# Kernel tuning notes

Measured on AMD Instinct MI355X. Metric: run time of the kernel, lower is better.

The kernel has to match this reference:

```python
import jax, jax.numpy as jnp
import numpy as np

B, L, D, H, U = 1024, 256, 256, 512, 512


def setup_inputs() -> dict:
    key = jax.random.key(0)
    ks = jax.random.split(key, 5)
    scale_f = 1.0
    return {
        "features": jax.random.normal(ks[0], (B, L, D), dtype=jnp.float32),
        "hidden": jax.random.normal(ks[1], (B, H), dtype=jnp.float32),
        "W1": jax.random.normal(ks[2], (D, U), dtype=jnp.float32) / np.sqrt(D),
        "b1": jnp.zeros((U,), dtype=jnp.float32),
        "W2": jax.random.normal(ks[3], (H, U), dtype=jnp.float32) / np.sqrt(H),
        "b2": jnp.zeros((U,), dtype=jnp.float32),
        "Wv": jax.random.normal(ks[4], (U, 1), dtype=jnp.float32) / np.sqrt(U),
        "bv": jnp.zeros((1,), dtype=jnp.float32),
    }


def reference(features, hidden, W1, b1, W2, b2, Wv, bv):
    # features: [B, L, D], hidden: [B, H]
    proj_f = jnp.einsum("bld,du->blu", features, W1) + b1      # [B, L, U]
    proj_h = (hidden @ W2 + b2)[:, None, :]                      # [B, 1, U]
    score = jnp.tanh(proj_f + proj_h)                            # [B, L, U]
    logits = jnp.einsum("blu,uo->blo", score, Wv) + bv           # [B, L, 1]
    attention_weights = jax.nn.softmax(logits, axis=1)           # [B, L, 1]
    context_vector = jnp.sum(attention_weights * features, axis=1)  # [B, D]
    return (context_vector, attention_weights)
```

## Files before the change

### kernel.cpp

```cpp
#include <hip/hip_runtime.h>
#include <hip/hip_bf16.h>

#define B_ 1024
#define L_ 256
#define D_ 256
#define H_ 512
#define U_ 512
#define M_ (B_ * L_)

#define BM 128
#define BN 128
#define BK 64

typedef float f32x4 __attribute__((ext_vector_type(4)));
typedef short bf16x8 __attribute__((ext_vector_type(8)));

__device__ __forceinline__ short f2bf(float f) {
  unsigned u = __float_as_uint(f);
  u += 0x7fffu + ((u >> 16) & 1u);
  return (short)(u >> 16);
}

__device__ __forceinline__ void load16_g2l(const void* g, void* l) {
  __builtin_amdgcn_global_load_lds(
      (const __attribute__((address_space(1))) unsigned int*)g,
      (__attribute__((address_space(3))) unsigned int*)l, 16, 0, 0);
}

__device__ __forceinline__ float fast_tanh(float x) {
  float e = __expf(2.0f * x);
  return 1.0f - 2.0f * __builtin_amdgcn_rcpf(e + 1.0f);
}

__global__ void k_w1t(const float* __restrict__ W1, short* __restrict__ W1T) {
  int idx = blockIdx.x * 256 + threadIdx.x;
  int u = idx >> 8;
  int d = idx & 255;
  W1T[idx] = f2bf(W1[(size_t)d * U_ + u]);
}

__global__ void k_projh(const float* __restrict__ hidden, const float* __restrict__ W2,
                        const float* __restrict__ b1, const float* __restrict__ b2,
                        float* __restrict__ ph) {
  int u = blockIdx.x * 256 + threadIdx.x;
  int b0 = blockIdx.y * 8;
  float acc[8] = {0.f, 0.f, 0.f, 0.f, 0.f, 0.f, 0.f, 0.f};
  for (int h = 0; h < H_; ++h) {
    float w = W2[(size_t)h * U_ + u];
#pragma unroll
    for (int i = 0; i < 8; ++i) acc[i] = fmaf(hidden[(size_t)(b0 + i) * H_ + h], w, acc[i]);
  }
  float bias = b1[u] + b2[u];
#pragma unroll
  for (int i = 0; i < 8; ++i) ph[(size_t)(b0 + i) * U_ + u] = acc[i] + bias;
}

__global__ __launch_bounds__(256, 3) void k_gemm(
    const float* __restrict__ F,
    const short* __restrict__ W1T,
    const float* __restrict__ ph,
    const float* __restrict__ Wv,
    float* __restrict__ logits) {
  __shared__ __align__(16) short As[BM * BK];
  __shared__ __align__(16) short Bs[2][BN * BK];

  const int tid = threadIdx.x;
  const int lane = tid & 63;
  const int hi = lane >> 4;
  const int wid = tid >> 6;
  const int wr = wid >> 1, wc = wid & 1;
  const int tile = ((blockIdx.x & 7) << 10) | (blockIdx.x >> 3);
  const int ntile = tile & 3;
  const int mtile = tile >> 2;
  const int m0 = mtile * BM;
  const int n0 = ntile * BN;
  const int b = m0 >> 8;

  const bf16x8* As8 = (const bf16x8*)As;

  const float* agp[4];
  int aslot[4];
  const short* bgp[4];
#pragma unroll
  for (int i = 0; i < 4; ++i) {
    int s = i * 256 + tid;
    int arow = s >> 3;
    int akq = (s & 7) ^ (arow & 7);
    agp[i] = F + (size_t)(m0 + arow) * D_ + akq * 8;
    aslot[i] = s;
    bgp[i] = W1T + (size_t)(n0 + arow) * D_ + akq * 8;
  }

  f32x4 acc[4][4];
  const f32x4 fz = {0.f, 0.f, 0.f, 0.f};
#pragma unroll
  for (int mi = 0; mi < 4; ++mi)
#pragma unroll
    for (int ni = 0; ni < 4; ++ni) acc[mi][ni] = fz;

  f32x4 ar[4][2];
#pragma unroll
  for (int i = 0; i < 4; ++i) {
    ar[i][0] = *(const f32x4*)(agp[i]);
    ar[i][1] = *(const f32x4*)(agp[i] + 4);
    agp[i] += BK;
  }
#pragma unroll
  for (int i = 0; i < 4; ++i) {
    load16_g2l(bgp[i], &Bs[0][(size_t)(i * 256 + tid) * 8]);
    bgp[i] += BK;
  }

  for (int kt = 0; kt < 4; ++kt) {
    const bf16x8* BsC = (const bf16x8*)Bs[kt & 1];
    __syncthreads();
#pragma unroll
    for (int i = 0; i < 4; ++i) {
      bf16x8 w;
#pragma unroll
      for (int j = 0; j < 4; ++j) { w[j] = f2bf(ar[i][0][j]); w[4 + j] = f2bf(ar[i][1][j]); }
      ((bf16x8*)As)[aslot[i]] = w;
    }
    __syncthreads();
    if (kt < 3) {
#pragma unroll
      for (int i = 0; i < 4; ++i) {
        ar[i][0] = *(const f32x4*)(agp[i]);
        ar[i][1] = *(const f32x4*)(agp[i] + 4);
        agp[i] += BK;
      }
#pragma unroll
      for (int i = 0; i < 4; ++i) {
        load16_g2l(bgp[i], &Bs[(kt + 1) & 1][(size_t)(i * 256 + tid) * 8]);
        bgp[i] += BK;
      }
    }

#pragma unroll
    for (int kk = 0; kk < 2; ++kk) {
      bf16x8 af[4], bfr[4];
#pragma unroll
      for (int mi = 0; mi < 4; ++mi) {
        int rA = wr * 64 + mi * 16 + (lane & 15);
        af[mi] = As8[rA * 8 + ((kk * 4 + hi) ^ (rA & 7))];
      }
#pragma unroll
      for (int ni = 0; ni < 4; ++ni) {
        int nB = wc * 64 + ni * 16 + (lane & 15);
        bfr[ni] = BsC[nB * 8 + ((kk * 4 + hi) ^ (nB & 7))];
      }
#pragma unroll
      for (int mi = 0; mi < 4; ++mi)
#pragma unroll
        for (int ni = 0; ni < 4; ++ni)
          acc[mi][ni] = __builtin_amdgcn_mfma_f32_16x16x32_bf16(af[mi], bfr[ni], acc[mi][ni], 0, 0, 0);
    }
  }

  const float* phr = ph + (size_t)b * U_;
  float phv[4], wvv[4];
#pragma unroll
  for (int ni = 0; ni < 4; ++ni) {
    int u = n0 + wc * 64 + ni * 16 + (lane & 15);
    phv[ni] = phr[u];
    wvv[ni] = Wv[u];
  }
#pragma unroll
  for (int mi = 0; mi < 4; ++mi) {
    float cs[4] = {0.f, 0.f, 0.f, 0.f};
#pragma unroll
    for (int ni = 0; ni < 4; ++ni) {
#pragma unroll
      for (int r = 0; r < 4; ++r) {
        float x = acc[mi][ni][r] + phv[ni];
        cs[r] += fast_tanh(x) * wvv[ni];
      }
    }
#pragma unroll
    for (int off = 1; off < 16; off <<= 1) {
#pragma unroll
      for (int r = 0; r < 4; ++r) cs[r] += __shfl_xor(cs[r], off);
    }
    if ((lane & 15) == 0) {
      int g = m0 + wr * 64 + mi * 16 + ((lane >> 4) << 2);
#pragma unroll
      for (int r = 0; r < 4; ++r) atomicAdd(&logits[g + r], cs[r]);
    }
  }
}

__global__ void k_smctx(const float* __restrict__ logits, const float* __restrict__ F,
                        float* __restrict__ outw, float* __restrict__ ctx) {
  __shared__ float wl[L_];
  __shared__ f32x4 part[256];
  __shared__ float red[8];
  int b = blockIdx.x, t = threadIdx.x;
  float x = logits[(size_t)b * L_ + t];
  float m = x;
#pragma unroll
  for (int off = 32; off >= 1; off >>= 1) m = fmaxf(m, __shfl_xor(m, off));
  if ((t & 63) == 0) red[t >> 6] = m;
  __syncthreads();
  m = fmaxf(fmaxf(red[0], red[1]), fmaxf(red[2], red[3]));
  float e = __expf(x - m);
  float s = e;
#pragma unroll
  for (int off = 32; off >= 1; off >>= 1) s += __shfl_xor(s, off);
  if ((t & 63) == 0) red[4 + (t >> 6)] = s;
  __syncthreads();
  s = (red[4] + red[5]) + (red[6] + red[7]);
  float w = e / s;
  outw[(size_t)b * L_ + t] = w;
  wl[t] = w;
  __syncthreads();

  int lq = t >> 6, dq = t & 63;
  const f32x4* F4 = (const f32x4*)(F + (size_t)b * L_ * D_);
  f32x4 acc = {0.f, 0.f, 0.f, 0.f};
  for (int l = lq; l < L_; l += 4) acc += wl[l] * F4[l * 64 + dq];
  part[t] = acc;
  __syncthreads();
  if (lq == 0) {
    f32x4 r = (part[t] + part[t + 64]) + (part[t + 128] + part[t + 192]);
    ((f32x4*)ctx)[(size_t)b * 64 + dq] = r;
  }
}

extern "C" void kernel_launch(void* const* d_in, const int* in_sizes, int n_in,
                              void* d_out, int out_size, void* d_ws, size_t ws_size,
                              hipStream_t stream) {
  const float* F      = (const float*)d_in[0];
  const float* hidden = (const float*)d_in[1];
  const float* W1     = (const float*)d_in[2];
  const float* b1     = (const float*)d_in[3];
  const float* W2     = (const float*)d_in[4];
  const float* b2     = (const float*)d_in[5];
  const float* Wv     = (const float*)d_in[6];

  float* out_ctx = (float*)d_out;
  float* out_w   = out_ctx + (size_t)B_ * D_;

  char* ws = (char*)d_ws;
  short* W1T   = (short*)ws;
  float* ph    = (float*)(ws + 262144);
  float* logits = (float*)(ws + 262144 + 2097152);

  hipMemsetAsync(logits, 0, (size_t)M_ * sizeof(float), stream);
  k_w1t<<<512, 256, 0, stream>>>(W1, W1T);
  k_projh<<<dim3(2, 128), 256, 0, stream>>>(hidden, W2, b1, b2, ph);
  k_gemm<<<8192, 256, 0, stream>>>(F, W1T, ph, Wv, logits);
  k_smctx<<<1024, 256, 0, stream>>>(logits, F, out_w, out_ctx);
}
```

Measured before the change: 236.5 us.

## Pre-cast features to bf16 in a separate pass and load GEMM A tiles via direct-to-LDS

Adds a kernel that converts the full fp32 feature tensor to bf16 in workspace. The GEMM then loads both A and B tiles with global_load_lds, drops register staging and the in-kernel conversion, and single-buffers B so it can run at higher occupancy (launch bounds 4). In exchange it adds an extra full read of F plus a bf16 write and re-read (about 128 MB and 64 MB of traffic), and the K loop no longer prefetches the next tile. The old kernel is kept as a fallback when the workspace is too small for the bf16 copy.

```diff
diff --git a/kernel.cpp b/kernel.cpp
--- a/kernel.cpp
+++ b/kernel.cpp
@@ -14,6 +14,7 @@
 
 typedef float f32x4 __attribute__((ext_vector_type(4)));
 typedef short bf16x8 __attribute__((ext_vector_type(8)));
+typedef short bf16x4 __attribute__((ext_vector_type(4)));
 
 __device__ __forceinline__ short f2bf(float f) {
   unsigned u = __float_as_uint(f);
@@ -37,6 +38,19 @@
   int u = idx >> 8;
   int d = idx & 255;
   W1T[idx] = f2bf(W1[(size_t)d * U_ + u]);
+}
+
+__global__ void k_cast(const float* __restrict__ F, short* __restrict__ Fbf) {
+  size_t i = ((size_t)blockIdx.x * 256 + threadIdx.x) * 4;
+  const size_t stride = (size_t)4096 * 256 * 4;
+#pragma unroll
+  for (int it = 0; it < 16; ++it, i += stride) {
+    f32x4 v = *(const f32x4*)(F + i);
+    bf16x4 w;
+#pragma unroll
+    for (int j = 0; j < 4; ++j) w[j] = f2bf(v[j]);
+    *(bf16x4*)(Fbf + i) = w;
+  }
 }
 
 __global__ void k_projh(const float* __restrict__ hidden, const float* __restrict__ W2,
@@ -55,14 +69,14 @@
   for (int i = 0; i < 8; ++i) ph[(size_t)(b0 + i) * U_ + u] = acc[i] + bias;
 }
 
-__global__ __launch_bounds__(256, 3) void k_gemm(
-    const float* __restrict__ F,
+__global__ __launch_bounds__(256, 4) void k_gemm(
+    const short* __restrict__ Fbf,
     const short* __restrict__ W1T,
     const float* __restrict__ ph,
     const float* __restrict__ Wv,
     float* __restrict__ logits) {
   __shared__ __align__(16) short As[BM * BK];
-  __shared__ __align__(16) short Bs[2][BN * BK];
+  __shared__ __align__(16) short Bs[BN * BK];
 
   const int tid = threadIdx.x;
   const int lane = tid & 63;
@@ -77,6 +91,113 @@
   const int b = m0 >> 8;
 
   const bf16x8* As8 = (const bf16x8*)As;
+  const bf16x8* Bs8 = (const bf16x8*)Bs;
+
+  const short* agp[4];
+  const short* bgp[4];
+#pragma unroll
+  for (int i = 0; i < 4; ++i) {
+    int s = i * 256 + tid;
+    int row = s >> 3;
+    int kq = (s & 7) ^ (row & 7);
+    agp[i] = Fbf + (size_t)(m0 + row) * D_ + kq * 8;
+    bgp[i] = W1T + (size_t)(n0 + row) * D_ + kq * 8;
+  }
+
+  f32x4 acc[4][4];
+  const f32x4 fz = {0.f, 0.f, 0.f, 0.f};
+#pragma unroll
+  for (int mi = 0; mi < 4; ++mi)
+#pragma unroll
+    for (int ni = 0; ni < 4; ++ni) acc[mi][ni] = fz;
+
+  for (int kt = 0; kt < 4; ++kt) {
+    if (kt) __syncthreads();
+#pragma unroll
+    for (int i = 0; i < 4; ++i) {
+      load16_g2l(agp[i], &As[(size_t)(i * 256 + tid) * 8]);
+      agp[i] += BK;
+    }
+#pragma unroll
+    for (int i = 0; i < 4; ++i) {
+      load16_g2l(bgp[i], &Bs[(size_t)(i * 256 + tid) * 8]);
+      bgp[i] += BK;
+    }
+    __syncthreads();
+
+#pragma unroll
+    for (int kk = 0; kk < 2; ++kk) {
+      bf16x8 af[4], bfr[4];
+#pragma unroll
+      for (int mi = 0; mi < 4; ++mi) {
+        int rA = wr * 64 + mi * 16 + (lane & 15);
+        af[mi] = As8[rA * 8 + ((kk * 4 + hi) ^ (rA & 7))];
+      }
+#pragma unroll
+      for (int ni = 0; ni < 4; ++ni) {
+        int nB = wc * 64 + ni * 16 + (lane & 15);
+        bfr[ni] = Bs8[nB * 8 + ((kk * 4 + hi) ^ (nB & 7))];
+      }
+#pragma unroll
+      for (int mi = 0; mi < 4; ++mi)
+#pragma unroll
+        for (int ni = 0; ni < 4; ++ni)
+          acc[mi][ni] = __builtin_amdgcn_mfma_f32_16x16x32_bf16(af[mi], bfr[ni], acc[mi][ni], 0, 0, 0);
+    }
+  }
+
+  const float* phr = ph + (size_t)b * U_;
+  float phv[4], wvv[4];
+#pragma unroll
+  for (int ni = 0; ni < 4; ++ni) {
+    int u = n0 + wc * 64 + ni * 16 + (lane & 15);
+    phv[ni] = phr[u];
+    wvv[ni] = Wv[u];
+  }
+#pragma unroll
+  for (int mi = 0; mi < 4; ++mi) {
+    float cs[4] = {0.f, 0.f, 0.f, 0.f};
+#pragma unroll
+    for (int ni = 0; ni < 4; ++ni) {
+#pragma unroll
+      for (int r = 0; r < 4; ++r) {
+        float x = acc[mi][ni][r] + phv[ni];
+        cs[r] += fast_tanh(x) * wvv[ni];
+      }
+    }
+#pragma unroll
+    for (int off = 1; off < 16; off <<= 1) {
+#pragma unroll
+      for (int r = 0; r < 4; ++r) cs[r] += __shfl_xor(cs[r], off);
+    }
+    if ((lane & 15) == 0) {
+      int g = m0 + wr * 64 + mi * 16 + ((lane >> 4) << 2);
+#pragma unroll
+      for (int r = 0; r < 4; ++r) atomicAdd(&logits[g + r], cs[r]);
+    }
+  }
+}
+
+__global__ __launch_bounds__(256, 3) void k_gemm_fb(
+    const float* __restrict__ F, const short* __restrict__ W1T,
+    const float* __restrict__ ph, const float* __restrict__ Wv,
+    float* __restrict__ logits) {
+  __shared__ __align__(16) short As[BM * BK];
+  __shared__ __align__(16) short Bs[2][BN * BK];
+
+  const int tid = threadIdx.x;
+  const int lane = tid & 63;
+  const int hi = lane >> 4;
+  const int wid = tid >> 6;
+  const int wr = wid >> 1, wc = wid & 1;
+  const int tile = ((blockIdx.x & 7) << 10) | (blockIdx.x >> 3);
+  const int ntile = tile & 3;
+  const int mtile = tile >> 2;
+  const int m0 = mtile * BM;
+  const int n0 = ntile * BN;
+  const int b = m0 >> 8;
+
+  const bf16x8* As8 = (const bf16x8*)As;
 
   const float* agp[4];
   int aslot[4];
@@ -135,7 +256,6 @@
         bgp[i] += BK;
       }
     }
-
 #pragma unroll
     for (int kk = 0; kk < 2; ++kk) {
       bf16x8 af[4], bfr[4];
@@ -241,13 +361,21 @@
   float* out_w   = out_ctx + (size_t)B_ * D_;
 
   char* ws = (char*)d_ws;
-  short* W1T   = (short*)ws;
-  float* ph    = (float*)(ws + 262144);
+  short* W1T    = (short*)ws;
+  float* ph     = (float*)(ws + 262144);
   float* logits = (float*)(ws + 262144 + 2097152);
+  const size_t fb_off = 262144 + 2097152 + 1048576;
+  short* Fbf    = (short*)(ws + fb_off);
+  const bool fast = ws_size >= fb_off + (size_t)M_ * D_ * sizeof(short);
 
   hipMemsetAsync(logits, 0, (size_t)M_ * sizeof(float), stream);
   k_w1t<<<512, 256, 0, stream>>>(W1, W1T);
   k_projh<<<dim3(2, 128), 256, 0, stream>>>(hidden, W2, b1, b2, ph);
-  k_gemm<<<8192, 256, 0, stream>>>(F, W1T, ph, Wv, logits);
+  if (fast) {
+    k_cast<<<4096, 256, 0, stream>>>(F, Fbf);
+    k_gemm<<<8192, 256, 0, stream>>>(Fbf, W1T, ph, Wv, logits);
+  } else {
+    k_gemm_fb<<<8192, 256, 0, stream>>>(F, W1T, ph, Wv, logits);
+  }
   k_smctx<<<1024, 256, 0, stream>>>(logits, F, out_w, out_ctx);
 }
```

Result: slower. 295.8 us (+25.0%).
